# Kernel optimization log

Hardware: AMD Instinct MI355X
Metric: run time of the kernel (lower is better)

## Reference

```python
import jax, jax.numpy as jnp
import numpy as np

N_HEADS = 16
KQ_DIM = 64
EMB_DIM = 1024
CTX_DIM = 1024
EPS = 1e-5

def _layernorm(x, w, b):
    # LayerNorm over last dim (kq_dim), elementwise affine
    mu = jnp.mean(x, axis=-1, keepdims=True)
    var = jnp.mean(jnp.square(x - mu), axis=-1, keepdims=True)
    return (x - mu) * jax.lax.rsqrt(var + EPS) * w + b

def setup_inputs() -> dict:
    key = jax.random.key(0)
    ks = jax.random.split(key, 10)
    B, SQ, SK = 2, 2048, 2048
    inner = N_HEADS * KQ_DIM
    s_e = 1.0 / np.sqrt(EMB_DIM)
    s_c = 1.0 / np.sqrt(CTX_DIM)
    s_i = 1.0 / np.sqrt(inner)
    return {
        "emb": jax.random.normal(ks[0], (B, SQ, EMB_DIM), jnp.float32),
        "context": jax.random.normal(ks[1], (B, SK, CTX_DIM), jnp.float32),
        "Wq": jax.random.uniform(ks[2], (inner, EMB_DIM), jnp.float32, -s_e, s_e),
        "Wk": jax.random.uniform(ks[3], (inner, CTX_DIM), jnp.float32, -s_c, s_c),
        "Wv": jax.random.uniform(ks[4], (inner, CTX_DIM), jnp.float32, -s_c, s_c),
        "Wu": jax.random.uniform(ks[5], (EMB_DIM, inner), jnp.float32, -s_i, s_i),
        "bu": jax.random.uniform(ks[6], (EMB_DIM,), jnp.float32, -s_i, s_i),
        "qn_w": jnp.ones((KQ_DIM,), jnp.float32),
        "qn_b": jnp.zeros((KQ_DIM,), jnp.float32),
        "kn_w": jnp.ones((KQ_DIM,), jnp.float32),
        "kn_b": jnp.zeros((KQ_DIM,), jnp.float32),
    }

def reference(emb, context, Wq, Wk, Wv, Wu, bu, qn_w, qn_b, kn_w, kn_b):
    B, SQ, _ = emb.shape
    SK = context.shape[1]
    # projections (no bias), reshape to [B, H, S, D]
    q = (emb @ Wq.T).reshape(B, SQ, N_HEADS, KQ_DIM).transpose(0, 2, 1, 3)
    k = (context @ Wk.T).reshape(B, SK, N_HEADS, KQ_DIM).transpose(0, 2, 1, 3)
    v = (context @ Wv.T).reshape(B, SK, N_HEADS, KQ_DIM).transpose(0, 2, 1, 3)
    q = _layernorm(q, qn_w, qn_b)
    k = _layernorm(k, kn_w, kn_b)
    scale = 1.0 / jnp.sqrt(jnp.asarray(KQ_DIM, emb.dtype))
    attn = jnp.einsum('bhqd,bhkd->bhqk', q, k) * scale
    attn = jax.nn.softmax(attn, axis=-1)
    out = jnp.einsum('bhqk,bhkd->bhqd', attn, v)
    out = out.transpose(0, 2, 1, 3).reshape(B, SQ, N_HEADS * KQ_DIM)
    return out @ Wu.T + bu
```

## Files before the change

kernel.cpp:

```cpp
#include <hip/hip_runtime.h>


typedef __attribute__((ext_vector_type(8)))  short bf16x8;
typedef __attribute__((ext_vector_type(4)))  short bf16x4;
typedef __attribute__((ext_vector_type(4)))  float f32x4;
typedef __attribute__((ext_vector_type(16))) float f32x16;
typedef __attribute__((ext_vector_type(4)))  unsigned int u32x4;

#define SM_SCALE 0.18033688f

typedef __attribute__((address_space(1))) const void cg_void;
typedef __attribute__((address_space(3))) void lds_void_t;

__device__ __forceinline__ void gl_lds16(const void* g, void* l){
  __builtin_amdgcn_global_load_lds((cg_void*)g, (lds_void_t*)l, 16, 0, 0);
}

__device__ __forceinline__ short f2b(float f){
  unsigned int u;
  __builtin_memcpy(&u, &f, 4);
  u += 0x7fffu + ((u >> 16) & 1u);
  return (short)(u >> 16);
}

__global__ __launch_bounds__(256) void cvt6_kernel(
    const float* __restrict__ emb, const float* __restrict__ ctx,
    const float* __restrict__ Wq, const float* __restrict__ Wk,
    const float* __restrict__ Wv, const float* __restrict__ Wu,
    short* __restrict__ o_emb, short* __restrict__ o_ctx,
    short* __restrict__ o_wq, short* __restrict__ o_wk,
    short* __restrict__ o_wv, short* __restrict__ o_wu)
{
  const long M1 = 1024L * 1024L, M4 = 4L * M1;
  long e = ((long)blockIdx.x * 256 + threadIdx.x) * 4;
  if (e >= 12L * M1) return;
  const float* src; short* dst; long off;
  if      (e <     M4)      { src = emb; dst = o_emb; off = e;           }
  else if (e < 2 * M4)      { src = ctx; dst = o_ctx; off = e - M4;      }
  else if (e < 2 * M4 + M1) { src = Wq;  dst = o_wq;  off = e - 2 * M4;  }
  else if (e < 2 * M4 + 2*M1){src = Wk;  dst = o_wk;  off = e - 2*M4 - M1;}
  else if (e < 2 * M4 + 3*M1){src = Wv;  dst = o_wv;  off = e - 2*M4 - 2*M1;}
  else                      { src = Wu;  dst = o_wu;  off = e - 2*M4 - 3*M1;}
  f32x4 v = *(const f32x4*)(src + off);
  bf16x4 o;
  o[0] = f2b(v[0]); o[1] = f2b(v[1]); o[2] = f2b(v[2]); o[3] = f2b(v[3]);
  *(bf16x4*)(dst + off) = o;
}

__global__ __launch_bounds__(256) void gemm_qkv_kernel(
    const short* __restrict__ embh, const short* __restrict__ ctxh,
    const short* __restrict__ Wqh, const short* __restrict__ Wkh,
    const short* __restrict__ Wvh,
    short* __restrict__ qo, short* __restrict__ ko, short* __restrict__ vto,
    const float* __restrict__ qw, const float* __restrict__ qb,
    const float* __restrict__ kw, const float* __restrict__ kb)
{
  const int K = 1024;
  __shared__ short As[128 * 64];
  __shared__ short Bs[128 * 64];
  const int tid  = threadIdx.x;
  const int wave = tid >> 6, lane = tid & 63;
  const int quad = lane >> 4, r16 = lane & 15;
  const int wm = (wave >> 1) * 64, wn = (wave & 1) * 64;

  const int task = blockIdx.y;
  int bn, bm, N;
  const short *A, *B;
  if (task == 2){
    bn = (blockIdx.x & 31) * 128; bm = (blockIdx.x >> 5) * 128; N = 4096;
    A = Wvh; B = ctxh;
  } else {
    bm = (blockIdx.x & 31) * 128; bn = (blockIdx.x >> 5) * 128; N = 1024;
    A = task ? ctxh : embh; B = task ? Wkh : Wqh;
  }

  f32x4 acc[4][4];
#pragma unroll
  for (int i = 0; i < 4; i++)
#pragma unroll
    for (int j = 0; j < 4; j++)
      acc[i][j] = (f32x4){0.f, 0.f, 0.f, 0.f};

  const int sr7 = (lane >> 3) & 7;
  const size_t arow = (size_t)(bm + wave * 8 + (lane >> 3)) * K
                      + (((lane & 7) ^ sr7) * 8);
  const size_t brow = (size_t)(bn + wave * 8 + (lane >> 3)) * K
                      + (((lane & 7) ^ sr7) * 8);
  const int sw = ((quad ^ (r16 & 7)) << 3);

  for (int k0 = 0; k0 < K; k0 += 64){
#pragma unroll
    for (int i = 0; i < 4; i++){
      gl_lds16(A + arow + (size_t)32 * i * K + k0, &As[wave * 512 + i * 2048]);
      gl_lds16(B + brow + (size_t)32 * i * K + k0, &Bs[wave * 512 + i * 2048]);
    }
    __syncthreads();
#pragma unroll
    for (int kk = 0; kk < 2; kk++){
      const int off = sw ^ (kk << 5);
      bf16x8 af[4], bq[4];
#pragma unroll
      for (int i = 0; i < 4; i++)
        af[i] = *(const bf16x8*)(&As[(wm + i*16 + r16) * 64 + off]);
#pragma unroll
      for (int j = 0; j < 4; j++)
        bq[j] = *(const bf16x8*)(&Bs[(wn + j*16 + r16) * 64 + off]);
#pragma unroll
      for (int i = 0; i < 4; i++)
#pragma unroll
        for (int j = 0; j < 4; j++)
          acc[i][j] = __builtin_amdgcn_mfma_f32_16x16x32_bf16(af[i], bq[j], acc[i][j], 0, 0, 0);
    }
    __syncthreads();
  }

  if (task < 2){
    short* Ch = task ? ko : qo;
    const float* lw = task ? kw : qw;
    const float* lb = task ? kb : qb;
    const float post = task ? 1.0f : SM_SCALE;
    float wv[4], bv[4];
#pragma unroll
    for (int j = 0; j < 4; j++){
      wv[j] = lw[j*16 + r16] * post;
      bv[j] = lb[j*16 + r16] * post;
    }
#pragma unroll
    for (int i = 0; i < 4; i++){
#pragma unroll
      for (int t = 0; t < 4; t++){
        float a[4];
#pragma unroll
        for (int j = 0; j < 4; j++) a[j] = acc[i][j][t];
        float s = a[0] + a[1] + a[2] + a[3];
        s += __shfl_xor(s, 1); s += __shfl_xor(s, 2);
        s += __shfl_xor(s, 4); s += __shfl_xor(s, 8);
        const float mu = s * 0.015625f;
        float d[4], sq = 0.f;
#pragma unroll
        for (int j = 0; j < 4; j++){ d[j] = a[j] - mu; sq += d[j]*d[j]; }
        sq += __shfl_xor(sq, 1); sq += __shfl_xor(sq, 2);
        sq += __shfl_xor(sq, 4); sq += __shfl_xor(sq, 8);
        const float si = rsqrtf(sq * 0.015625f + 1e-5f);
        const size_t row = (size_t)(bm + wm + i*16 + quad*4 + t);
#pragma unroll
        for (int j = 0; j < 4; j++)
          Ch[row * 1024 + (bn + wn + j*16 + r16)] = f2b(d[j] * si * wv[j] + bv[j]);
      }
    }
  } else {
#pragma unroll
    for (int i = 0; i < 4; i++){
#pragma unroll
      for (int j = 0; j < 4; j++){
        const int p = (r16 & 3) | ((j & 1) << 2) | (((r16 >> 2) & 1) << 3)
                      | (((r16 >> 3) & 1) << 4);
        const int col = ((bn + wn + j*16 + r16) & ~31) | p;
#pragma unroll
        for (int t = 0; t < 4; t++){
          const size_t row = (size_t)(bm + wm + i*16 + quad*4 + t);
          vto[row * (size_t)N + col] = f2b(acc[i][j][t]);
        }
      }
    }
  }
}

__global__ __launch_bounds__(1024, 4) void gemm_out_kernel(
    const short* __restrict__ A, const short* __restrict__ B,
    float* __restrict__ Cf, const float* __restrict__ bias)
{
  const int K = 1024, N = 1024;
  __shared__ short As[4][128 * 64];
  __shared__ short Bs[4][128 * 64];
  const int tid  = threadIdx.x;
  const int wave = tid >> 6, lane = tid & 63;
  const int qt = wave >> 2, wg = wave & 3;
  const int quad = lane >> 4, r16 = lane & 15;
  const int wm = (wg >> 1) * 64, wn = (wg & 1) * 64;
  const int bm = blockIdx.x * 128, bn = blockIdx.y * 128;

  f32x4 acc[4][4];
#pragma unroll
  for (int i = 0; i < 4; i++)
#pragma unroll
    for (int j = 0; j < 4; j++)
      acc[i][j] = (f32x4){0.f, 0.f, 0.f, 0.f};

  const int kh = qt * 256;
  const int sr7 = (lane >> 3) & 7;
  const size_t arow = (size_t)(bm + wg * 8 + (lane >> 3)) * K + kh
                      + (((lane & 7) ^ sr7) * 8);
  const size_t brow = (size_t)(bn + wg * 8 + (lane >> 3)) * K + kh
                      + (((lane & 7) ^ sr7) * 8);
  const int sw = ((quad ^ (r16 & 7)) << 3);

  for (int k0 = 0; k0 < 256; k0 += 64){
#pragma unroll
    for (int i = 0; i < 4; i++){
      gl_lds16(A + arow + (size_t)32 * i * K + k0, &As[qt][wg * 512 + i * 2048]);
      gl_lds16(B + brow + (size_t)32 * i * K + k0, &Bs[qt][wg * 512 + i * 2048]);
    }
    __syncthreads();
#pragma unroll
    for (int kk = 0; kk < 2; kk++){
      const int off = sw ^ (kk << 5);
      bf16x8 af[4], bq[4];
#pragma unroll
      for (int i = 0; i < 4; i++)
        af[i] = *(const bf16x8*)(&As[qt][(wm + i*16 + r16) * 64 + off]);
#pragma unroll
      for (int j = 0; j < 4; j++)
        bq[j] = *(const bf16x8*)(&Bs[qt][(wn + j*16 + r16) * 64 + off]);
#pragma unroll
      for (int i = 0; i < 4; i++)
#pragma unroll
        for (int j = 0; j < 4; j++)
          acc[i][j] = __builtin_amdgcn_mfma_f32_16x16x32_bf16(af[i], bq[j], acc[i][j], 0, 0, 0);
    }
    __syncthreads();
  }

  float* scr = (float*)&As[0][0];
#pragma unroll
  for (int i = 0; i < 4; i++){
    if (qt != 0){
      float* p = scr + ((qt - 1) * 256 + wg * 64 + lane) * 17;
#pragma unroll
      for (int j = 0; j < 4; j++)
#pragma unroll
        for (int t = 0; t < 4; t++) p[j*4 + t] = acc[i][j][t];
    }
    __syncthreads();
    if (qt == 0){
      const float* p0 = scr + (wg * 64 + lane) * 17;
      const float* p1 = p0 + 256 * 17;
      const float* p2 = p1 + 256 * 17;
#pragma unroll
      for (int j = 0; j < 4; j++){
        const int col = bn + wn + j*16 + r16;
#pragma unroll
        for (int t = 0; t < 4; t++){
          const size_t row = (size_t)(bm + wm + i*16 + quad*4 + t);
          Cf[row * N + col] = acc[i][j][t] + p0[j*4+t] + p1[j*4+t] + p2[j*4+t]
                              + bias[col];
        }
      }
    }
    __syncthreads();
  }
}

__global__ __launch_bounds__(512, 4) void flash2_kernel(
    const short* __restrict__ Q, const short* __restrict__ K,
    const short* __restrict__ Vt, short* __restrict__ O)
{
  __shared__ __align__(16) long long smem8[8192];
  short* Ks  = (short*)smem8;
  short* Vts = Ks + 16384;
  float* scr = (float*)smem8;

  const int tid = threadIdx.x;
  const int wave = tid >> 6, lane = tid & 63;
  const int half = wave >> 2, wg = wave & 3;
  const int hh = lane >> 5, q5 = lane & 31;
  const int h = blockIdx.x, qb = blockIdx.y, b = blockIdx.z;
  const int q0 = qb * 128 + wg * 32;

  const size_t kbase = ((size_t)b * 2048) * 1024 + (size_t)h * 64;
  const size_t vbase = ((size_t)h * 64) * 4096 + (size_t)b * 2048;

  bf16x8 qf[4];
  {
    const size_t qrow = ((size_t)b * 2048 + q0 + q5) * 1024 + (size_t)h * 64;
#pragma unroll
    for (int c = 0; c < 4; c++)
      qf[c] = *(const bf16x8*)(Q + qrow + c * 16 + hh * 8);
  }

  f32x16 oacc[2];
#pragma unroll
  for (int mt = 0; mt < 2; mt++)
#pragma unroll
    for (int t = 0; t < 16; t++) oacc[mt][t] = 0.f;
  float lsum = 0.f;

  const int srow = lane >> 3;
  const int csrc = ((lane & 7) ^ srow) * 8;
  const int wr0 = wg * 16;

#define STAGE(bufi, kt)                                                         \
  {                                                                             \
    const short* ks = K + kbase + (size_t)((kt) * 64 + wr0 + srow) * 1024 + csrc; \
    const short* vs = Vt + vbase + (size_t)(wr0 + srow) * 4096 + (kt) * 64 + csrc; \
    short* kd = Ks  + (half * 2 + (bufi)) * 4096 + wr0 * 64;                    \
    short* vd = Vts + (half * 2 + (bufi)) * 4096 + wr0 * 64;                    \
    gl_lds16(ks,            kd);                                                \
    gl_lds16(ks + 8 * 1024, kd + 512);                                          \
    gl_lds16(vs,            vd);                                                \
    gl_lds16(vs + 8 * 4096, vd + 512);                                          \
  }

  STAGE(0, half)

  for (int i = 0; i < 16; i++){
    const int buf = i & 1;
    __syncthreads();
    if (i + 1 < 16) STAGE(buf ^ 1, 2 * (i + 1) + half)

    const short* kb_l = Ks  + (half * 2 + buf) * 4096;
    const short* vb_l = Vts + (half * 2 + buf) * 4096;

    bf16x8 kf[2][4];
#pragma unroll
    for (int s32 = 0; s32 < 2; s32++){
      const int key = s32 * 32 + q5;
#pragma unroll
      for (int c = 0; c < 4; c++)
        kf[s32][c] = *(const bf16x8*)(&kb_l[key * 64 + (((2*c + hh) ^ (key & 7)) << 3)]);
    }
    f32x16 sacc[2];
#pragma unroll
    for (int t = 0; t < 16; t++){ sacc[0][t] = 0.f; sacc[1][t] = 0.f; }
#pragma unroll
    for (int c = 0; c < 4; c++){
      sacc[0] = __builtin_amdgcn_mfma_f32_32x32x16_bf16(kf[0][c], qf[c], sacc[0], 0, 0, 0);
      sacc[1] = __builtin_amdgcn_mfma_f32_32x32x16_bf16(kf[1][c], qf[c], sacc[1], 0, 0, 0);
    }

#pragma unroll
    for (int s32 = 0; s32 < 2; s32++){
      unsigned int pu[16];
#pragma unroll
      for (int t = 0; t < 16; t++){
        const float e = __builtin_amdgcn_exp2f(sacc[s32][t]);
        lsum += e;
        unsigned int u; __builtin_memcpy(&u, &e, 4);
        pu[t] = u + 0x8000u;
      }

#pragma unroll
      for (int c = 0; c < 2; c++){
        u32x4 tmp;
        tmp[0] = __builtin_amdgcn_perm(pu[4*c + 1], pu[4*c + 0], 0x07060302u);
        tmp[1] = __builtin_amdgcn_perm(pu[4*c + 3], pu[4*c + 2], 0x07060302u);
        tmp[2] = __builtin_amdgcn_perm(pu[8 + 4*c + 1], pu[8 + 4*c + 0], 0x07060302u);
        tmp[3] = __builtin_amdgcn_perm(pu[8 + 4*c + 3], pu[8 + 4*c + 2], 0x07060302u);
        bf16x8 pf; __builtin_memcpy(&pf, &tmp, 16);
#pragma unroll
        for (int mt = 0; mt < 2; mt++){
          const int d = mt * 32 + q5;
          bf16x8 vf = *(const bf16x8*)(&vb_l[d * 64 + (((s32*4 + 2*c + hh) ^ (d & 7)) << 3)]);
          oacc[mt] = __builtin_amdgcn_mfma_f32_32x32x16_bf16(vf, pf, oacc[mt], 0, 0, 0);
        }
      }
    }
  }

  lsum += __shfl_xor(lsum, 32);
  __syncthreads();
  float* base = scr + (wg * 64 + lane) * 33;
  if (half == 1){
#pragma unroll
    for (int t = 0; t < 16; t++){ base[t] = oacc[0][t]; base[16 + t] = oacc[1][t]; }
    scr[8448 + wg * 64 + lane] = lsum;
  }
  __syncthreads();
  if (half == 0){
    const float l2 = scr[8448 + wg * 64 + lane];
    const float linv = 1.0f / (lsum + l2);
    const size_t orow = ((size_t)b * 2048 + q0 + q5) * 1024 + (size_t)h * 64;
#pragma unroll
    for (int mt = 0; mt < 2; mt++){
#pragma unroll
      for (int g = 0; g < 4; g++){
        bf16x4 o4;
#pragma unroll
        for (int u = 0; u < 4; u++)
          o4[u] = f2b((oacc[mt][g*4 + u] + base[mt*16 + g*4 + u]) * linv);
        *(bf16x4*)(O + orow + mt*32 + g*8 + 4*hh) = o4;
      }
    }
  }
}
#undef STAGE

extern "C" void kernel_launch(void* const* d_in, const int* in_sizes, int n_in,
                              void* d_out, int out_size, void* d_ws, size_t ws_size,
                              hipStream_t stream) {
  const float* emb  = (const float*)d_in[0];
  const float* ctx  = (const float*)d_in[1];
  const float* Wq   = (const float*)d_in[2];
  const float* Wk   = (const float*)d_in[3];
  const float* Wv   = (const float*)d_in[4];
  const float* Wu   = (const float*)d_in[5];
  const float* bu   = (const float*)d_in[6];
  const float* qn_w = (const float*)d_in[7];
  const float* qn_b = (const float*)d_in[8];
  const float* kn_w = (const float*)d_in[9];
  const float* kn_b = (const float*)d_in[10];
  float* out = (float*)d_out;

  const size_t BIG = (size_t)4096 * 1024;
  const size_t WSZ = (size_t)1024 * 1024;
  short* ws   = (short*)d_ws;
  short* embh = ws;
  short* ctxh = embh + BIG;
  short* Wqh  = ctxh + BIG;
  short* Wkh  = Wqh + WSZ;
  short* Wvh  = Wkh + WSZ;
  short* Wuh  = Wvh + WSZ;
  short* qh   = Wuh + WSZ;
  short* kh   = qh + BIG;
  short* vth  = kh + BIG;
  short* aoh  = vth + BIG;

  cvt6_kernel<<<12288, 256, 0, stream>>>(emb, ctx, Wq, Wk, Wv, Wu,
                                         embh, ctxh, Wqh, Wkh, Wvh, Wuh);

  gemm_qkv_kernel<<<dim3(256, 3), 256, 0, stream>>>(
      embh, ctxh, Wqh, Wkh, Wvh, qh, kh, vth,
      qn_w, qn_b, kn_w, kn_b);

  flash2_kernel<<<dim3(16, 16, 2), 512, 0, stream>>>(qh, kh, vth, aoh);

  gemm_out_kernel<<<dim3(32, 8), 1024, 0, stream>>>(aoh, Wuh, out, bu);
}
```

Measured before the change: 199.8 us.

## Shrink GEMM tiles for more blocks and compute softmax row sums via MFMA

The QKV GEMM moves from 128x128 to 128x64 tiles, doubling the grid and hinting 5 blocks per CU. The output GEMM drops its four-way split-K with a cross-wave LDS reduction in favour of plain 64x64 tiles on 256-thread blocks, launched as a 64x16 grid. The flash kernel no longer sums exponentials per lane in scalar code; it runs an extra MFMA against a ones vector, so the rounded bf16 probabilities are summed on the matrix units. The smaller tiles give each block less data reuse, and the ones-MFMA adds matrix work in exchange for fewer VALU adds.

```diff
diff --git a/kernel.cpp b/kernel.cpp
--- a/kernel.cpp
+++ b/kernel.cpp
@@ -47,7 +47,7 @@
   *(bf16x4*)(dst + off) = o;
 }
 
-__global__ __launch_bounds__(256) void gemm_qkv_kernel(
+__global__ __launch_bounds__(256, 5) void gemm_qkv_kernel(
     const short* __restrict__ embh, const short* __restrict__ ctxh,
     const short* __restrict__ Wqh, const short* __restrict__ Wkh,
     const short* __restrict__ Wvh,
@@ -57,26 +57,26 @@
 {
   const int K = 1024;
   __shared__ short As[128 * 64];
-  __shared__ short Bs[128 * 64];
+  __shared__ short Bs[64 * 64];
   const int tid  = threadIdx.x;
   const int wave = tid >> 6, lane = tid & 63;
   const int quad = lane >> 4, r16 = lane & 15;
-  const int wm = (wave >> 1) * 64, wn = (wave & 1) * 64;
+  const int wm = wave * 32;
 
   const int task = blockIdx.y;
   int bn, bm, N;
   const short *A, *B;
   if (task == 2){
-    bn = (blockIdx.x & 31) * 128; bm = (blockIdx.x >> 5) * 128; N = 4096;
+    bn = (blockIdx.x & 63) * 64; bm = (blockIdx.x >> 6) * 128; N = 4096;
     A = Wvh; B = ctxh;
   } else {
-    bm = (blockIdx.x & 31) * 128; bn = (blockIdx.x >> 5) * 128; N = 1024;
+    bm = (blockIdx.x & 31) * 128; bn = (blockIdx.x >> 5) * 64; N = 1024;
     A = task ? ctxh : embh; B = task ? Wkh : Wqh;
   }
 
-  f32x4 acc[4][4];
-#pragma unroll
-  for (int i = 0; i < 4; i++)
+  f32x4 acc[2][4];
+#pragma unroll
+  for (int i = 0; i < 2; i++)
 #pragma unroll
     for (int j = 0; j < 4; j++)
       acc[i][j] = (f32x4){0.f, 0.f, 0.f, 0.f};
@@ -90,23 +90,24 @@
 
   for (int k0 = 0; k0 < K; k0 += 64){
 #pragma unroll
-    for (int i = 0; i < 4; i++){
+    for (int i = 0; i < 4; i++)
       gl_lds16(A + arow + (size_t)32 * i * K + k0, &As[wave * 512 + i * 2048]);
+#pragma unroll
+    for (int i = 0; i < 2; i++)
       gl_lds16(B + brow + (size_t)32 * i * K + k0, &Bs[wave * 512 + i * 2048]);
-    }
     __syncthreads();
 #pragma unroll
     for (int kk = 0; kk < 2; kk++){
       const int off = sw ^ (kk << 5);
-      bf16x8 af[4], bq[4];
-#pragma unroll
-      for (int i = 0; i < 4; i++)
+      bf16x8 af[2], bq[4];
+#pragma unroll
+      for (int i = 0; i < 2; i++)
         af[i] = *(const bf16x8*)(&As[(wm + i*16 + r16) * 64 + off]);
 #pragma unroll
       for (int j = 0; j < 4; j++)
-        bq[j] = *(const bf16x8*)(&Bs[(wn + j*16 + r16) * 64 + off]);
-#pragma unroll
-      for (int i = 0; i < 4; i++)
+        bq[j] = *(const bf16x8*)(&Bs[(j*16 + r16) * 64 + off]);
+#pragma unroll
+      for (int i = 0; i < 2; i++)
 #pragma unroll
         for (int j = 0; j < 4; j++)
           acc[i][j] = __builtin_amdgcn_mfma_f32_16x16x32_bf16(af[i], bq[j], acc[i][j], 0, 0, 0);
@@ -126,7 +127,7 @@
       bv[j] = lb[j*16 + r16] * post;
     }
 #pragma unroll
-    for (int i = 0; i < 4; i++){
+    for (int i = 0; i < 2; i++){
 #pragma unroll
       for (int t = 0; t < 4; t++){
         float a[4];
@@ -145,17 +146,17 @@
         const size_t row = (size_t)(bm + wm + i*16 + quad*4 + t);
 #pragma unroll
         for (int j = 0; j < 4; j++)
-          Ch[row * 1024 + (bn + wn + j*16 + r16)] = f2b(d[j] * si * wv[j] + bv[j]);
+          Ch[row * 1024 + (bn + j*16 + r16)] = f2b(d[j] * si * wv[j] + bv[j]);
       }
     }
   } else {
 #pragma unroll
-    for (int i = 0; i < 4; i++){
+    for (int i = 0; i < 2; i++){
 #pragma unroll
       for (int j = 0; j < 4; j++){
         const int p = (r16 & 3) | ((j & 1) << 2) | (((r16 >> 2) & 1) << 3)
                       | (((r16 >> 3) & 1) << 4);
-        const int col = ((bn + wn + j*16 + r16) & ~31) | p;
+        const int col = ((bn + j*16 + r16) & ~31) | p;
 #pragma unroll
         for (int t = 0; t < 4; t++){
           const size_t row = (size_t)(bm + wm + i*16 + quad*4 + t);
@@ -166,88 +167,70 @@
   }
 }
 
-__global__ __launch_bounds__(1024, 4) void gemm_out_kernel(
+__global__ __launch_bounds__(256, 4) void gemm_out_kernel(
     const short* __restrict__ A, const short* __restrict__ B,
     float* __restrict__ Cf, const float* __restrict__ bias)
 {
   const int K = 1024, N = 1024;
-  __shared__ short As[4][128 * 64];
-  __shared__ short Bs[4][128 * 64];
+  __shared__ short As[64 * 64];
+  __shared__ short Bs[64 * 64];
   const int tid  = threadIdx.x;
   const int wave = tid >> 6, lane = tid & 63;
-  const int qt = wave >> 2, wg = wave & 3;
   const int quad = lane >> 4, r16 = lane & 15;
-  const int wm = (wg >> 1) * 64, wn = (wg & 1) * 64;
-  const int bm = blockIdx.x * 128, bn = blockIdx.y * 128;
-
-  f32x4 acc[4][4];
-#pragma unroll
-  for (int i = 0; i < 4; i++)
-#pragma unroll
-    for (int j = 0; j < 4; j++)
+  const int wm = (wave >> 1) * 32, wn = (wave & 1) * 32;
+  const int bm = blockIdx.x * 64, bn = blockIdx.y * 64;
+
+  f32x4 acc[2][2];
+#pragma unroll
+  for (int i = 0; i < 2; i++)
+#pragma unroll
+    for (int j = 0; j < 2; j++)
       acc[i][j] = (f32x4){0.f, 0.f, 0.f, 0.f};
 
-  const int kh = qt * 256;
   const int sr7 = (lane >> 3) & 7;
-  const size_t arow = (size_t)(bm + wg * 8 + (lane >> 3)) * K + kh
+  const size_t arow = (size_t)(bm + wave * 8 + (lane >> 3)) * K
                       + (((lane & 7) ^ sr7) * 8);
-  const size_t brow = (size_t)(bn + wg * 8 + (lane >> 3)) * K + kh
+  const size_t brow = (size_t)(bn + wave * 8 + (lane >> 3)) * K
                       + (((lane & 7) ^ sr7) * 8);
   const int sw = ((quad ^ (r16 & 7)) << 3);
 
-  for (int k0 = 0; k0 < 256; k0 += 64){
-#pragma unroll
-    for (int i = 0; i < 4; i++){
-      gl_lds16(A + arow + (size_t)32 * i * K + k0, &As[qt][wg * 512 + i * 2048]);
-      gl_lds16(B + brow + (size_t)32 * i * K + k0, &Bs[qt][wg * 512 + i * 2048]);
+  for (int k0 = 0; k0 < K; k0 += 64){
+#pragma unroll
+    for (int i = 0; i < 2; i++){
+      gl_lds16(A + arow + (size_t)32 * i * K + k0, &As[wave * 512 + i * 2048]);
+      gl_lds16(B + brow + (size_t)32 * i * K + k0, &Bs[wave * 512 + i * 2048]);
     }
     __syncthreads();
 #pragma unroll
     for (int kk = 0; kk < 2; kk++){
       const int off = sw ^ (kk << 5);
-      bf16x8 af[4], bq[4];
-#pragma unroll
-      for (int i = 0; i < 4; i++)
-        af[i] = *(const bf16x8*)(&As[qt][(wm + i*16 + r16) * 64 + off]);
-#pragma unroll
-      for (int j = 0; j < 4; j++)
-        bq[j] = *(const bf16x8*)(&Bs[qt][(wn + j*16 + r16) * 64 + off]);
-#pragma unroll
-      for (int i = 0; i < 4; i++)
-#pragma unroll
-        for (int j = 0; j < 4; j++)
+      bf16x8 af[2], bq[2];
+#pragma unroll
+      for (int i = 0; i < 2; i++)
+        af[i] = *(const bf16x8*)(&As[(wm + i*16 + r16) * 64 + off]);
+#pragma unroll
+      for (int j = 0; j < 2; j++)
+        bq[j] = *(const bf16x8*)(&Bs[(wn + j*16 + r16) * 64 + off]);
+#pragma unroll
+      for (int i = 0; i < 2; i++)
+#pragma unroll
+        for (int j = 0; j < 2; j++)
           acc[i][j] = __builtin_amdgcn_mfma_f32_16x16x32_bf16(af[i], bq[j], acc[i][j], 0, 0, 0);
     }
     __syncthreads();
   }
 
-  float* scr = (float*)&As[0][0];
-#pragma unroll
-  for (int i = 0; i < 4; i++){
-    if (qt != 0){
-      float* p = scr + ((qt - 1) * 256 + wg * 64 + lane) * 17;
-#pragma unroll
-      for (int j = 0; j < 4; j++)
-#pragma unroll
-        for (int t = 0; t < 4; t++) p[j*4 + t] = acc[i][j][t];
-    }
-    __syncthreads();
-    if (qt == 0){
-      const float* p0 = scr + (wg * 64 + lane) * 17;
-      const float* p1 = p0 + 256 * 17;
-      const float* p2 = p1 + 256 * 17;
-#pragma unroll
-      for (int j = 0; j < 4; j++){
-        const int col = bn + wn + j*16 + r16;
-#pragma unroll
-        for (int t = 0; t < 4; t++){
-          const size_t row = (size_t)(bm + wm + i*16 + quad*4 + t);
-          Cf[row * N + col] = acc[i][j][t] + p0[j*4+t] + p1[j*4+t] + p2[j*4+t]
-                              + bias[col];
-        }
-      }
-    }
-    __syncthreads();
+#pragma unroll
+  for (int i = 0; i < 2; i++){
+#pragma unroll
+    for (int j = 0; j < 2; j++){
+      const int col = bn + wn + j*16 + r16;
+#pragma unroll
+      for (int t = 0; t < 4; t++){
+        const size_t row = (size_t)(bm + wm + i*16 + quad*4 + t);
+        Cf[row * N + col] = acc[i][j][t] + bias[col];
+      }
+    }
   }
 }
 
@@ -278,12 +261,13 @@
       qf[c] = *(const bf16x8*)(Q + qrow + c * 16 + hh * 8);
   }
 
-  f32x16 oacc[2];
-#pragma unroll
-  for (int mt = 0; mt < 2; mt++)
-#pragma unroll
-    for (int t = 0; t < 16; t++) oacc[mt][t] = 0.f;
-  float lsum = 0.f;
+  bf16x8 onesf;
+#pragma unroll
+  for (int j = 0; j < 8; j++) onesf[j] = (short)0x3F80;
+
+  f32x16 oacc[2], oaccl;
+#pragma unroll
+  for (int t = 0; t < 16; t++){ oacc[0][t] = 0.f; oacc[1][t] = 0.f; oaccl[t] = 0.f; }
 
   const int srow = lane >> 3;
   const int csrc = ((lane & 7) ^ srow) * 8;
@@ -334,7 +318,6 @@
 #pragma unroll
       for (int t = 0; t < 16; t++){
         const float e = __builtin_amdgcn_exp2f(sacc[s32][t]);
-        lsum += e;
         unsigned int u; __builtin_memcpy(&u, &e, 4);
         pu[t] = u + 0x8000u;
       }
@@ -353,22 +336,23 @@
           bf16x8 vf = *(const bf16x8*)(&vb_l[d * 64 + (((s32*4 + 2*c + hh) ^ (d & 7)) << 3)]);
           oacc[mt] = __builtin_amdgcn_mfma_f32_32x32x16_bf16(vf, pf, oacc[mt], 0, 0, 0);
         }
-      }
-    }
-  }
-
-  lsum += __shfl_xor(lsum, 32);
+        oaccl = __builtin_amdgcn_mfma_f32_32x32x16_bf16(onesf, pf, oaccl, 0, 0, 0);
+      }
+    }
+  }
+
+  const float lhalf = oaccl[0];
   __syncthreads();
   float* base = scr + (wg * 64 + lane) * 33;
   if (half == 1){
 #pragma unroll
     for (int t = 0; t < 16; t++){ base[t] = oacc[0][t]; base[16 + t] = oacc[1][t]; }
-    scr[8448 + wg * 64 + lane] = lsum;
+    scr[8448 + wg * 64 + lane] = lhalf;
   }
   __syncthreads();
   if (half == 0){
     const float l2 = scr[8448 + wg * 64 + lane];
-    const float linv = 1.0f / (lsum + l2);
+    const float linv = 1.0f / (lhalf + l2);
     const size_t orow = ((size_t)b * 2048 + q0 + q5) * 1024 + (size_t)h * 64;
 #pragma unroll
     for (int mt = 0; mt < 2; mt++){
@@ -418,11 +402,11 @@
   cvt6_kernel<<<12288, 256, 0, stream>>>(emb, ctx, Wq, Wk, Wv, Wu,
                                          embh, ctxh, Wqh, Wkh, Wvh, Wuh);
 
-  gemm_qkv_kernel<<<dim3(256, 3), 256, 0, stream>>>(
+  gemm_qkv_kernel<<<dim3(512, 3), 256, 0, stream>>>(
       embh, ctxh, Wqh, Wkh, Wvh, qh, kh, vth,
       qn_w, qn_b, kn_w, kn_b);
 
   flash2_kernel<<<dim3(16, 16, 2), 512, 0, stream>>>(qh, kh, vth, aoh);
 
-  gemm_out_kernel<<<dim3(32, 8), 1024, 0, stream>>>(aoh, Wuh, out, bu);
-}
+  gemm_out_kernel<<<dim3(64, 16), 256, 0, stream>>>(aoh, Wuh, out, bu);
+}
```

Measured after the change: 194.2 us. 2.8% less time.
